# Kernel optimization log

Measured on AMD Instinct MI355X. Metric: run time of the kernel, lower is better.

## Reference

```python
import jax, jax.numpy as jnp
import numpy as np
from itertools import combinations

DIM = 3
METRIC = np.array([1.0, 1.0, 1.0], dtype=np.float32)
KERNEL_SIZE = 7
C_IN, C_OUT = 32, 32
HIDDEN = 64
NUM_LAYERS = 4
N_GRID = KERNEL_SIZE ** DIM


def _build_cayley(dim, metric):
    blades = [()] + [c for r in range(1, dim + 1) for c in combinations(range(dim), r)]
    idx = {b: i for i, b in enumerate(blades)}
    n = len(blades)
    C = np.zeros((n, n, n), dtype=np.float32)
    for i, a in enumerate(blades):
        for j, b in enumerate(blades):
            arr = list(a) + list(b)
            sign = 1.0
            changed = True
            while changed:
                changed = False
                t = 0
                while t < len(arr) - 1:
                    if arr[t] == arr[t + 1]:
                        sign *= metric[arr[t]]
                        del arr[t:t + 2]
                        changed = True
                        break
                    if arr[t] > arr[t + 1]:
                        arr[t], arr[t + 1] = arr[t + 1], arr[t]
                        sign = -sign
                        changed = True
                    t += 1
            C[i, j, idx[tuple(arr)]] = sign
    grades = np.array([len(b) for b in blades])
    return C, grades

_C_LRO, GRADES = _build_cayley(DIM, METRIC)
CAYLEY = np.transpose(_C_LRO, (0, 2, 1))  # [left, out, right] (CEGNN convention)
N_BLADES = CAYLEY.shape[0]
N_GRADES = DIM + 1

# nonzero grade-triple paths of the Cayley tensor and blade-level path-id lookup
_gp = np.zeros((N_GRADES,) * 3, dtype=bool)
for a in range(N_GRADES):
    for b in range(N_GRADES):
        for c in range(N_GRADES):
            _gp[a, b, c] = np.any(CAYLEY[np.ix_(GRADES == a, GRADES == b, GRADES == c)] != 0)
PATHS = np.argwhere(_gp)
P = len(PATHS)
assert P == 20  # product_paths_sum for Cl(3,0)
_pid = -np.ones((N_GRADES,) * 3, dtype=np.int64)
for p, (a, b, c) in enumerate(PATHS):
    _pid[a, b, c] = p
BLADE_PID = _pid[GRADES[:, None, None], GRADES[None, :, None], GRADES[None, None, :]]
BLADE_PID = np.where(BLADE_PID < 0, P, BLADE_PID)  # P -> zero slot

# centered relative-position grid, (N, 1, dim)
_ax = np.arange(KERNEL_SIZE, dtype=np.float32) - (KERNEL_SIZE - 1) / 2.0
_grid = np.stack(np.meshgrid(*([_ax] * DIM), indexing='ij'), axis=-1).reshape(-1, DIM)
REL_POS = jnp.asarray(_grid[:, None, :])
CAYLEY_J = jnp.asarray(CAYLEY)
GRADE_ONEHOT = jnp.asarray((GRADES[:, None] == np.arange(N_GRADES)[None, :]).astype(np.float32))
FACTOR = 1.0 / np.sqrt(float(KERNEL_SIZE ** DIM))
BLADES_OF = {g: np.where(GRADES == g)[0] for g in range(N_GRADES)}


def embed_grade(x, g):
    out = jnp.zeros(x.shape[:-1] + (N_BLADES,), x.dtype)
    return out.at[..., BLADES_OF[g]].set(x)


def expand_paths(w):
    # (..., P) grade-path weights -> (..., B, B, B) blade-level weights
    wz = jnp.concatenate([w, jnp.zeros(w.shape[:-1] + (1,), w.dtype)], axis=-1)
    return wz[..., BLADE_PID]


def mv_linear(x, W, b):
    # grade-wise equivariant channel mixing; x: (N,Ci,B), W: (G,Co,Ci), bias on scalar blade
    y = jnp.einsum('boi,nib->nob', W[GRADES], x)
    return y.at[:, :, 0].add(b)


def mv_silu(x, a, b):
    # gate each grade by sigmoid of its (learned-scaled) squared norm
    qg = jnp.einsum('ncb,bg->ncg', x * x, GRADE_ONEHOT)
    gate = jax.nn.sigmoid(a * qg + b)
    return x * gate[:, :, GRADES]


def gp_layer(x, w):
    # fully-connected steerable geometric product; x: (N,C,B), w: (Co,C,P)
    wc = expand_paths(w) * CAYLEY_J  # (Co, C, B, B, B)
    y = jnp.einsum('nik,oikjm,nim->noj', x, wc, x)
    return y / np.sqrt(float(x.shape[1]))


def setup_inputs() -> dict:
    key = jax.random.key(0)
    ks = jax.random.split(key, 8)
    G, B, H, Pn = N_GRADES, N_BLADES, HIDDEN, P
    rn = lambda k, s, sc: jax.random.normal(k, s, dtype=jnp.float32) * sc
    ci1 = C_IN + 1
    return {
        'condition': rn(ks[0], (C_IN, B), 1.0),
        'rel_pos_sigma': jnp.ones((1, 1, 1), jnp.float32),
        'cayley_w': rn(ks[1], (C_OUT, C_IN, Pn), 1.0 / np.sqrt(C_IN)),
        'lin0_W': rn(ks[2], (G, H, ci1), 1.0 / np.sqrt(ci1)),
        'lin0_b': jnp.zeros((H,), jnp.float32),
        'act0_a': rn(ks[3], (H, G), 0.2),
        'act0_b': jnp.zeros((H, G), jnp.float32),
        'gps_w': rn(ks[4], (NUM_LAYERS, H, H, Pn), 0.5 / np.sqrt(H)),
        'lins_W': rn(ks[5], (NUM_LAYERS - 1, G, H, H), 1.0 / np.sqrt(H)),
        'lins_b': jnp.zeros((NUM_LAYERS - 1, H), jnp.float32),
        'acts_a': rn(ks[6], (NUM_LAYERS - 1, H, G), 0.2),
        'acts_b': jnp.zeros((NUM_LAYERS - 1, H, G), jnp.float32),
        'out_W': rn(ks[7], (G, C_OUT * C_IN, H), 1.0 / np.sqrt(H)),
        'out_b': jnp.zeros((C_OUT * C_IN,), jnp.float32),
        'shell_sigma': jnp.ones((1, C_OUT, C_IN, B), jnp.float32),
    }


def reference(condition, rel_pos_sigma, cayley_w, lin0_W, lin0_b, act0_a, act0_b,
              gps_w, lins_W, lins_b, acts_a, acts_b, out_W, out_b, shell_sigma):
    metric = jnp.asarray(METRIC)
    q = jnp.sum(metric * REL_POS * REL_POS, axis=-1, keepdims=True)  # (N,1,1)
    scalar = jnp.exp(-q / (2.0 * rel_pos_sigma ** 2))
    x = embed_grade(scalar, 0) + embed_grade(REL_POS, 1)  # (N,1,B)
    cond = jnp.broadcast_to(condition[None], (N_GRID,) + condition.shape)
    x = jnp.concatenate([x, cond], axis=1)  # (N, c_in+1, B)
    # kernel network: CEGNN blocks [MVLinear -> MVSiLU -> steerable geometric product]
    h = gp_layer(mv_silu(mv_linear(x, lin0_W, lin0_b), act0_a, act0_b), gps_w[0])
    for l in range(NUM_LAYERS - 1):
        h = gp_layer(mv_silu(mv_linear(h, lins_W[l], lins_b[l]), acts_a[l], acts_b[l]), gps_w[l + 1])
    k = mv_linear(h, out_W, out_b).reshape(N_GRID, C_OUT, C_IN, N_BLADES)
    # per-(c_out,c_in,blade) scalar radial shell
    shell = jnp.exp(-q.reshape(N_GRID, 1, 1, 1) / (shell_sigma ** 2))
    k = k * shell * FACTOR
    # kernel head: sparse weighted-Cayley contraction
    wc = expand_paths(cayley_w) * CAYLEY_J  # (c_out, c_in, B, B, B)
    K = jnp.einsum('noik,oiklm->olimn', k, wc)
    return K.reshape(C_OUT * N_BLADES, C_IN * N_BLADES, KERNEL_SIZE, KERNEL_SIZE, KERNEL_SIZE)
```

## Files before the change

kernel.cpp:

```cpp
#include <hip/hip_runtime.h>
#include <math.h>

#define NB 8
#define NGRID 343
#define HID 64
#define NPATH 20

struct Tab {
  int prod_idx[8][8];
  int prod_sgn[8][8];
  int pid[4][4][4];
  int grade[8];
  int kk_idx[8][8];
  int kk_sgn[8][8];
};

constexpr Tab make_tab() {
  Tab t{};
  int mask[8]  = {0,1,2,4,3,5,6,7};
  int idxof[8] = {0,1,2,4,3,5,6,7};
  for (int k = 0; k < 8; ++k) {
    int g = 0;
    for (int b = 0; b < 3; ++b) g += (mask[k] >> b) & 1;
    t.grade[k] = g;
  }
  for (int k = 0; k < 8; ++k)
    for (int m = 0; m < 8; ++m) {
      int A = mask[k], B = mask[m];
      t.prod_idx[k][m] = idxof[A ^ B];
      int c = 0;
      for (int i = 0; i < 3; ++i)
        if ((B >> i) & 1)
          for (int j = i + 1; j < 3; ++j)
            if ((A >> j) & 1) c++;
      t.prod_sgn[k][m] = (c & 1) ? -1 : 1;
    }
  int pc = 0;
  for (int a = 0; a < 4; ++a)
    for (int b = 0; b < 4; ++b)
      for (int c = 0; c < 4; ++c) {
        bool ok = false;
        for (int k = 0; k < 8; ++k)
          for (int m = 0; m < 8; ++m)
            if (t.grade[k] == a && t.grade[m] == c &&
                t.grade[t.prod_idx[k][m]] == b)
              ok = true;
        t.pid[a][b][c] = ok ? pc++ : NPATH;
      }
  for (int l = 0; l < 8; ++l)
    for (int m = 0; m < 8; ++m)
      for (int k = 0; k < 8; ++k)
        if (t.prod_idx[k][m] == l) {
          t.kk_idx[l][m] = k;
          t.kk_sgn[l][m] = t.prod_sgn[k][m];
        }
  return t;
}
constexpr Tab TB = make_tab();

#define OFF_LIN0T 0
#define OFF_LINST 8448
#define OFF_GPST  57600
#define OFF_OUTWT 385280
#define OFF_KWS   647424

__global__ void ccs_prep_kernel(const float* __restrict__ lin0_W,
                                const float* __restrict__ lins_W,
                                const float* __restrict__ gps_w,
                                const float* __restrict__ out_W,
                                float* __restrict__ ws) {
  const int TOT = 8448 + 49152 + 327680 + 262144;
  for (int d = blockIdx.x * blockDim.x + threadIdx.x; d < TOT;
       d += gridDim.x * blockDim.x) {
    float v;
    if (d < 8448) {
      int idx = d;
      int hh = idx & 63, ch = (idx >> 6) % 33, g = (idx >> 6) / 33;
      v = lin0_W[(g * 64 + hh) * 33 + ch];
    } else if (d < 8448 + 49152) {
      int idx = d - OFF_LINST;
      int hh = idx & 63, i = (idx >> 6) & 63, g = (idx >> 12) & 3, l = idx >> 14;
      v = lins_W[((l * 4 + g) * 64 + hh) * 64 + i];
    } else if (d < 8448 + 49152 + 327680) {
      int idx = d - OFF_GPST;
      int o = idx & 63, p = (idx >> 6) % 20, i = ((idx >> 6) / 20) & 63,
          l = idx / 81920;
      v = gps_w[((l * 64 + o) * 64 + i) * 20 + p];
    } else {
      int idx = d - OFF_OUTWT;
      int oc = idx & 1023, i = (idx >> 10) & 63, g = idx >> 16;
      v = out_W[(g * 1024 + oc) * 64 + i];
    }
    ws[d] = v;
  }
}

__launch_bounds__(512)
__global__ void ccs_net_kernel(const float* __restrict__ condition,
                               const float* __restrict__ rel_pos_sigma,
                               const float* __restrict__ lin0_b,
                               const float* __restrict__ act0_a,
                               const float* __restrict__ act0_b,
                               const float* __restrict__ lins_b,
                               const float* __restrict__ acts_a,
                               const float* __restrict__ acts_b,
                               const float* __restrict__ out_b,
                               const float* __restrict__ shell_sigma,
                               const float* __restrict__ ws,
                               float* __restrict__ kws) {
  const float* lin0t = ws + OFF_LIN0T;
  const float* linst = ws + OFF_LINST;
  const float* gpst  = ws + OFF_GPST;
  const float* outwt = ws + OFF_OUTWT;

  __shared__ float xb[33 * 8];
  __shared__ float x0r[2][8];
  __shared__ __align__(16) float F0[2 * 512];
  __shared__ __align__(16) float F1[2 * 512];
  __shared__ float part[2 * 8 * 8 * 64];

  const int tid = threadIdx.x;
  const int n0 = blockIdx.x * 2;
  const int n1 = n0 + 1;

  const float sig = rel_pos_sigma[0];

  float qq[2];
  {
    int iz = n0 % 7, iy = (n0 / 7) % 7, ix = n0 / 49;
    float px = (float)ix - 3.f, py = (float)iy - 3.f, pz = (float)iz - 3.f;
    qq[0] = px * px + py * py + pz * pz;
  }
  {
    int nc = (n1 < NGRID) ? n1 : (NGRID - 1);
    int iz = nc % 7, iy = (nc / 7) % 7, ix = nc / 49;
    float px = (float)ix - 3.f, py = (float)iy - 3.f, pz = (float)iz - 3.f;
    qq[1] = px * px + py * py + pz * pz;
  }

  for (int t = tid; t < 264; t += 512) {
    int ch = t >> 3, b = t & 7;
    xb[t] = (ch == 0) ? 0.f : condition[(ch - 1) * 8 + b];
  }
  if (tid < 16) {
    int pt = tid >> 3, b = tid & 7;
    int nc = n0 + pt;
    if (nc >= NGRID) nc = NGRID - 1;
    int iz = nc % 7, iy = (nc / 7) % 7, ix = nc / 49;
    float px = (float)ix - 3.f, py = (float)iy - 3.f, pz = (float)iz - 3.f;
    float q = px * px + py * py + pz * pz;
    float scal = expf(-q / (2.f * sig * sig));
    x0r[pt][b] =
        (b == 0) ? scal : (b == 1) ? px : (b == 2) ? py : (b == 3) ? pz : 0.f;
  }
  __syncthreads();

  const int b8 = tid & 7;
  const int hh = (tid >> 3) & 63;
  const int gb = TB.grade[b8];

  {
    const float* wrow = lin0t + gb * 33 * 64 + hh;
    float w0 = wrow[0];
    float a0 = w0 * x0r[0][b8];
    float a1 = w0 * x0r[1][b8];
    if (b8 == 0) {
      float bb = lin0_b[hh];
      a0 += bb;
      a1 += bb;
    }
    #pragma unroll
    for (int ch = 1; ch < 33; ++ch) {
      float w = wrow[ch * 64];
      float xv = xb[ch * 8 + b8];
      a0 = fmaf(w, xv, a0);
      a1 = fmaf(w, xv, a1);
    }
    F0[hh * 8 + b8] = a0;
    F0[512 + hh * 8 + b8] = a1;
  }
  __syncthreads();

  auto silu = [&](const float* src, float* dst, const float* aa,
                  const float* bb) {
    int s0 = (gb == 0) ? 0 : (gb == 1) ? 1 : (gb == 2) ? 4 : 7;
    int cnt = (gb == 0 || gb == 3) ? 1 : 3;
    float A = aa[hh * 4 + gb], B = bb[hh * 4 + gb];
    #pragma unroll
    for (int pt = 0; pt < 2; ++pt) {
      float qg = 0.f;
      for (int u = 0; u < cnt; ++u) {
        float v = src[pt * 512 + hh * 8 + s0 + u];
        qg = fmaf(v, v, qg);
      }
      float z = fmaf(A, qg, B);
      float gate = 1.f / (1.f + expf(-z));
      dst[pt * 512 + hh * 8 + b8] = src[pt * 512 + hh * 8 + b8] * gate;
    }
  };

  auto lin = [&](const float* src, float* dst, const float* wt,
                 const float* bias) {
    const float* wrow = wt + gb * 64 * 64 + hh;
    float a0 = 0.f, a1 = 0.f;
    if (b8 == 0) {
      float bb = bias[hh];
      a0 = bb;
      a1 = bb;
    }
    #pragma unroll
    for (int i = 0; i < 64; ++i) {
      float w = wrow[i * 64];
      a0 = fmaf(w, src[i * 8 + b8], a0);
      a1 = fmaf(w, src[512 + i * 8 + b8], a1);
    }
    dst[hh * 8 + b8] = a0;
    dst[512 + hh * 8 + b8] = a1;
  };

  auto gp = [&](const float* src, float* dst, const float* wl) {
    const int o = tid & 63;
    const int isub = tid >> 6;
    float fa[8], fb[8];
    #pragma unroll
    for (int j = 0; j < 8; ++j) {
      fa[j] = 0.f;
      fb[j] = 0.f;
    }
    for (int it = 0; it < 8; ++it) {
      int i = isub * 8 + it;
      float4 va0 = *(const float4*)(src + i * 8);
      float4 va1 = *(const float4*)(src + i * 8 + 4);
      float4 vb0 = *(const float4*)(src + 512 + i * 8);
      float4 vb1 = *(const float4*)(src + 512 + i * 8 + 4);
      float xA[8] = {va0.x, va0.y, va0.z, va0.w, va1.x, va1.y, va1.z, va1.w};
      float xB[8] = {vb0.x, vb0.y, vb0.z, vb0.w, vb1.x, vb1.y, vb1.z, vb1.w};
      const float* wb = wl + i * 20 * 64 + o;
      float wp[20];
      #pragma unroll
      for (int p = 0; p < 20; ++p) wp[p] = wb[p * 64];
      #pragma unroll
      for (int k = 0; k < 8; ++k) {
        #pragma unroll
        for (int m = 0; m < 8; ++m) {
          const int j = TB.prod_idx[k][m];
          const int p = TB.pid[TB.grade[k]][TB.grade[j]][TB.grade[m]];
          if (TB.prod_sgn[k][m] > 0) {
            fa[j] = fmaf(xA[k] * xA[m], wp[p], fa[j]);
            fb[j] = fmaf(xB[k] * xB[m], wp[p], fb[j]);
          } else {
            fa[j] = fmaf(-xA[k] * xA[m], wp[p], fa[j]);
            fb[j] = fmaf(-xB[k] * xB[m], wp[p], fb[j]);
          }
        }
      }
    }
    #pragma unroll
    for (int j = 0; j < 8; ++j) {
      part[isub * 512 + j * 64 + o] = fa[j];
      part[4096 + isub * 512 + j * 64 + o] = fb[j];
    }
    __syncthreads();
    #pragma unroll
    for (int r = 0; r < 2; ++r) {
      int item = tid + r * 512;
      int oo = item & 63;
      int j = (item >> 6) & 7;
      int pt = item >> 9;
      const float* pp = part + pt * 4096 + j * 64 + oo;
      float s = pp[0] + pp[512] + pp[1024] + pp[1536] + pp[2048] + pp[2560] +
                pp[3072] + pp[3584];
      dst[pt * 512 + oo * 8 + j] = s * 0.125f;
    }
    __syncthreads();
  };

  silu(F0, F1, act0_a, act0_b);
  __syncthreads();
  gp(F1, F0, gpst + 0);

  float* f = F0;
  float* g_ = F1;
  for (int l = 0; l < 3; ++l) {
    lin(f, g_, linst + l * 16384, lins_b + l * 64);
    __syncthreads();
    silu(g_, f, acts_a + l * 256, acts_b + l * 256);
    __syncthreads();
    gp(f, g_, gpst + (l + 1) * 81920);
    float* t = f; f = g_; g_ = t;
  }

  const float FACTOR = 1.0f / sqrtf(343.0f);
  #pragma unroll
  for (int r = 0; r < 2; ++r) {
    int oc = tid + r * 512;
    float acc[2][8];
    #pragma unroll
    for (int pt = 0; pt < 2; ++pt)
      #pragma unroll
      for (int b = 0; b < 8; ++b) acc[pt][b] = 0.f;
    {
      float bb = out_b[oc];
      acc[0][0] = bb;
      acc[1][0] = bb;
    }
    #pragma unroll 4
    for (int i = 0; i < 64; ++i) {
      float w0 = outwt[(0 * 64 + i) * 1024 + oc];
      float w1 = outwt[(1 * 64 + i) * 1024 + oc];
      float w2 = outwt[(2 * 64 + i) * 1024 + oc];
      float w3 = outwt[(3 * 64 + i) * 1024 + oc];
      #pragma unroll
      for (int pt = 0; pt < 2; ++pt) {
        float4 h0 = *(const float4*)(f + pt * 512 + i * 8);
        float4 h1 = *(const float4*)(f + pt * 512 + i * 8 + 4);
        acc[pt][0] = fmaf(w0, h0.x, acc[pt][0]);
        acc[pt][1] = fmaf(w1, h0.y, acc[pt][1]);
        acc[pt][2] = fmaf(w1, h0.z, acc[pt][2]);
        acc[pt][3] = fmaf(w1, h0.w, acc[pt][3]);
        acc[pt][4] = fmaf(w2, h1.x, acc[pt][4]);
        acc[pt][5] = fmaf(w2, h1.y, acc[pt][5]);
        acc[pt][6] = fmaf(w2, h1.z, acc[pt][6]);
        acc[pt][7] = fmaf(w3, h1.w, acc[pt][7]);
      }
    }
    #pragma unroll
    for (int pt = 0; pt < 2; ++pt) {
      int n = n0 + pt;
      if (n < NGRID) {
        float q = qq[pt];
        float out8[8];
        #pragma unroll
        for (int b = 0; b < 8; ++b) {
          float ss = shell_sigma[oc * 8 + b];
          out8[b] = acc[pt][b] * expf(-q / (ss * ss)) * FACTOR;
        }
        float4* dstp = (float4*)(kws + ((size_t)oc * 343 + n) * 8);
        dstp[0] = make_float4(out8[0], out8[1], out8[2], out8[3]);
        dstp[1] = make_float4(out8[4], out8[5], out8[6], out8[7]);
      }
    }
  }
}

__launch_bounds__(64)
__global__ void ccs_expand_kernel(const float* __restrict__ cayley_w,
                                  const float* __restrict__ kws,
                                  float* __restrict__ out) {
  const int oi = blockIdx.x;
  const int o = oi >> 5, i = oi & 31;
  const int n = blockIdx.y * 64 + threadIdx.x;
  if (n >= NGRID) return;
  float cw[20];
  #pragma unroll
  for (int p = 0; p < 20; ++p) cw[p] = cayley_w[oi * 20 + p];
  const float* kp = kws + ((size_t)oi * 343 + n) * 8;
  float k8[8];
  #pragma unroll
  for (int b = 0; b < 8; ++b) k8[b] = kp[b];
  #pragma unroll
  for (int l = 0; l < 8; ++l) {
    #pragma unroll
    for (int m = 0; m < 8; ++m) {
      const int kk = TB.kk_idx[l][m];
      const int p = TB.pid[TB.grade[kk]][TB.grade[l]][TB.grade[m]];
      float v = k8[kk] * cw[p];
      if (TB.kk_sgn[l][m] < 0) v = -v;
      out[((size_t)((o * 8 + l) * 256 + i * 8 + m)) * 343 + n] = v;
    }
  }
}

extern "C" void kernel_launch(void* const* d_in, const int* in_sizes, int n_in,
                              void* d_out, int out_size, void* d_ws,
                              size_t ws_size, hipStream_t stream) {
  const float* condition     = (const float*)d_in[0];
  const float* rel_pos_sigma = (const float*)d_in[1];
  const float* cayley_w      = (const float*)d_in[2];
  const float* lin0_W        = (const float*)d_in[3];
  const float* lin0_b        = (const float*)d_in[4];
  const float* act0_a        = (const float*)d_in[5];
  const float* act0_b        = (const float*)d_in[6];
  const float* gps_w         = (const float*)d_in[7];
  const float* lins_W        = (const float*)d_in[8];
  const float* lins_b        = (const float*)d_in[9];
  const float* acts_a        = (const float*)d_in[10];
  const float* acts_b        = (const float*)d_in[11];
  const float* out_W         = (const float*)d_in[12];
  const float* out_b         = (const float*)d_in[13];
  const float* shell_sigma   = (const float*)d_in[14];

  float* ws = (float*)d_ws;
  float* kws = ws + OFF_KWS;
  float* out = (float*)d_out;

  ccs_prep_kernel<<<dim3(640), dim3(256), 0, stream>>>(lin0_W, lins_W, gps_w,
                                                       out_W, ws);
  ccs_net_kernel<<<dim3((NGRID + 1) / 2), dim3(512), 0, stream>>>(
      condition, rel_pos_sigma, lin0_b, act0_a, act0_b, lins_b, acts_a, acts_b,
      out_b, shell_sigma, ws, kws);
  ccs_expand_kernel<<<dim3(1024, 6), dim3(64), 0, stream>>>(cayley_w, kws, out);
}
```

Baseline: 229.8 us.

## Read weights in native layout with vectorized loads instead of transposing in prep

The prep kernel no longer transposes lins_W, gps_w and out_W into workspace; the net kernel reads them in their original row-major layout with float4 loads. This removes most of the prep kernel's traffic. A transposed copy of the activations (FT) is kept in shared memory so the linear layer can do float4 dot products per thread. The gp weights are double-buffered across iterations, and the output projection now handles two output channels per thread with vectorized weight loads. In exchange, lanes now read strided rows instead of coalesced columns, and there is extra shared-memory traffic and register pressure.

```diff
diff --git a/kernel.cpp b/kernel.cpp
--- a/kernel.cpp
+++ b/kernel.cpp
@@ -59,40 +59,14 @@
 constexpr Tab TB = make_tab();
 
 #define OFF_LIN0T 0
-#define OFF_LINST 8448
-#define OFF_GPST  57600
-#define OFF_OUTWT 385280
-#define OFF_KWS   647424
+#define OFF_KWS   9216
 
 __global__ void ccs_prep_kernel(const float* __restrict__ lin0_W,
-                                const float* __restrict__ lins_W,
-                                const float* __restrict__ gps_w,
-                                const float* __restrict__ out_W,
                                 float* __restrict__ ws) {
-  const int TOT = 8448 + 49152 + 327680 + 262144;
-  for (int d = blockIdx.x * blockDim.x + threadIdx.x; d < TOT;
-       d += gridDim.x * blockDim.x) {
-    float v;
-    if (d < 8448) {
-      int idx = d;
-      int hh = idx & 63, ch = (idx >> 6) % 33, g = (idx >> 6) / 33;
-      v = lin0_W[(g * 64 + hh) * 33 + ch];
-    } else if (d < 8448 + 49152) {
-      int idx = d - OFF_LINST;
-      int hh = idx & 63, i = (idx >> 6) & 63, g = (idx >> 12) & 3, l = idx >> 14;
-      v = lins_W[((l * 4 + g) * 64 + hh) * 64 + i];
-    } else if (d < 8448 + 49152 + 327680) {
-      int idx = d - OFF_GPST;
-      int o = idx & 63, p = (idx >> 6) % 20, i = ((idx >> 6) / 20) & 63,
-          l = idx / 81920;
-      v = gps_w[((l * 64 + o) * 64 + i) * 20 + p];
-    } else {
-      int idx = d - OFF_OUTWT;
-      int oc = idx & 1023, i = (idx >> 10) & 63, g = idx >> 16;
-      v = out_W[(g * 1024 + oc) * 64 + i];
-    }
-    ws[d] = v;
-  }
+  int d = blockIdx.x * blockDim.x + threadIdx.x;
+  if (d >= 9216) return;
+  int ch = d % 36, hh = (d / 36) & 63, g = d / 2304;
+  ws[d] = (ch < 33) ? lin0_W[(g * 64 + hh) * 33 + ch] : 0.f;
 }
 
 __launch_bounds__(512)
@@ -106,17 +80,18 @@
                                const float* __restrict__ acts_b,
                                const float* __restrict__ out_b,
                                const float* __restrict__ shell_sigma,
+                               const float* __restrict__ lins_W,
+                               const float* __restrict__ gps_w,
+                               const float* __restrict__ out_W,
                                const float* __restrict__ ws,
                                float* __restrict__ kws) {
   const float* lin0t = ws + OFF_LIN0T;
-  const float* linst = ws + OFF_LINST;
-  const float* gpst  = ws + OFF_GPST;
-  const float* outwt = ws + OFF_OUTWT;
 
   __shared__ float xb[33 * 8];
   __shared__ float x0r[2][8];
   __shared__ __align__(16) float F0[2 * 512];
   __shared__ __align__(16) float F1[2 * 512];
+  __shared__ __align__(16) float FT[2 * 512];
   __shared__ float part[2 * 8 * 8 * 64];
 
   const int tid = threadIdx.x;
@@ -160,10 +135,12 @@
   const int gb = TB.grade[b8];
 
   {
-    const float* wrow = lin0t + gb * 33 * 64 + hh;
-    float w0 = wrow[0];
-    float a0 = w0 * x0r[0][b8];
-    float a1 = w0 * x0r[1][b8];
+    const float4* w4 = (const float4*)(lin0t + (gb * 64 + hh) * 36);
+    float wv[36];
+    #pragma unroll
+    for (int t2 = 0; t2 < 9; ++t2) ((float4*)wv)[t2] = w4[t2];
+    float a0 = wv[0] * x0r[0][b8];
+    float a1 = wv[0] * x0r[1][b8];
     if (b8 == 0) {
       float bb = lin0_b[hh];
       a0 += bb;
@@ -171,10 +148,9 @@
     }
     #pragma unroll
     for (int ch = 1; ch < 33; ++ch) {
-      float w = wrow[ch * 64];
       float xv = xb[ch * 8 + b8];
-      a0 = fmaf(w, xv, a0);
-      a1 = fmaf(w, xv, a1);
+      a0 = fmaf(wv[ch], xv, a0);
+      a1 = fmaf(wv[ch], xv, a1);
     }
     F0[hh * 8 + b8] = a0;
     F0[512 + hh * 8 + b8] = a1;
@@ -199,9 +175,10 @@
     }
   };
 
-  auto lin = [&](const float* src, float* dst, const float* wt,
-                 const float* bias) {
-    const float* wrow = wt + gb * 64 * 64 + hh;
+  auto lin = [&](float* dst, const float* wt, const float* bias) {
+    const float4* w4 = (const float4*)(wt + gb * 4096 + hh * 64);
+    const float4* sA = (const float4*)(FT + b8 * 64);
+    const float4* sB = (const float4*)(FT + 512 + b8 * 64);
     float a0 = 0.f, a1 = 0.f;
     if (b8 == 0) {
       float bb = bias[hh];
@@ -209,10 +186,16 @@
       a1 = bb;
     }
     #pragma unroll
-    for (int i = 0; i < 64; ++i) {
-      float w = wrow[i * 64];
-      a0 = fmaf(w, src[i * 8 + b8], a0);
-      a1 = fmaf(w, src[512 + i * 8 + b8], a1);
+    for (int i4 = 0; i4 < 16; ++i4) {
+      float wv[4], xa[4], xbv[4];
+      *(float4*)wv = w4[i4];
+      *(float4*)xa = sA[i4];
+      *(float4*)xbv = sB[i4];
+      #pragma unroll
+      for (int u = 0; u < 4; ++u) {
+        a0 = fmaf(wv[u], xa[u], a0);
+        a1 = fmaf(wv[u], xbv[u], a1);
+      }
     }
     dst[hh * 8 + b8] = a0;
     dst[512 + hh * 8 + b8] = a1;
@@ -227,7 +210,19 @@
       fa[j] = 0.f;
       fb[j] = 0.f;
     }
+    const float4* wb4 =
+        (const float4*)(wl + (size_t)o * 1280 + (size_t)isub * 160);
+    float4 wq[5];
+    #pragma unroll
+    for (int t2 = 0; t2 < 5; ++t2) wq[t2] = wb4[t2];
+    #pragma unroll
     for (int it = 0; it < 8; ++it) {
+      float4 wn[5];
+      if (it < 7) {
+        const float4* nb = wb4 + (it + 1) * 5;
+        #pragma unroll
+        for (int t2 = 0; t2 < 5; ++t2) wn[t2] = nb[t2];
+      }
       int i = isub * 8 + it;
       float4 va0 = *(const float4*)(src + i * 8);
       float4 va1 = *(const float4*)(src + i * 8 + 4);
@@ -235,10 +230,9 @@
       float4 vb1 = *(const float4*)(src + 512 + i * 8 + 4);
       float xA[8] = {va0.x, va0.y, va0.z, va0.w, va1.x, va1.y, va1.z, va1.w};
       float xB[8] = {vb0.x, vb0.y, vb0.z, vb0.w, vb1.x, vb1.y, vb1.z, vb1.w};
-      const float* wb = wl + i * 20 * 64 + o;
       float wp[20];
       #pragma unroll
-      for (int p = 0; p < 20; ++p) wp[p] = wb[p * 64];
+      for (int t2 = 0; t2 < 5; ++t2) ((float4*)wp)[t2] = wq[t2];
       #pragma unroll
       for (int k = 0; k < 8; ++k) {
         #pragma unroll
@@ -254,6 +248,10 @@
           }
         }
       }
+      if (it < 7) {
+        #pragma unroll
+        for (int t2 = 0; t2 < 5; ++t2) wq[t2] = wn[t2];
+      }
     }
     #pragma unroll
     for (int j = 0; j < 8; ++j) {
@@ -270,74 +268,94 @@
       const float* pp = part + pt * 4096 + j * 64 + oo;
       float s = pp[0] + pp[512] + pp[1024] + pp[1536] + pp[2048] + pp[2560] +
                 pp[3072] + pp[3584];
-      dst[pt * 512 + oo * 8 + j] = s * 0.125f;
+      s *= 0.125f;
+      dst[pt * 512 + oo * 8 + j] = s;
+      FT[pt * 512 + j * 64 + oo] = s;
     }
     __syncthreads();
   };
 
   silu(F0, F1, act0_a, act0_b);
   __syncthreads();
-  gp(F1, F0, gpst + 0);
+  gp(F1, F0, gps_w + 0);
 
   float* f = F0;
   float* g_ = F1;
   for (int l = 0; l < 3; ++l) {
-    lin(f, g_, linst + l * 16384, lins_b + l * 64);
+    lin(g_, lins_W + l * 16384, lins_b + l * 64);
     __syncthreads();
     silu(g_, f, acts_a + l * 256, acts_b + l * 256);
     __syncthreads();
-    gp(f, g_, gpst + (l + 1) * 81920);
+    gp(f, g_, gps_w + (size_t)(l + 1) * 81920);
     float* t = f; f = g_; g_ = t;
   }
 
   const float FACTOR = 1.0f / sqrtf(343.0f);
-  #pragma unroll
-  for (int r = 0; r < 2; ++r) {
-    int oc = tid + r * 512;
-    float acc[2][8];
-    #pragma unroll
-    for (int pt = 0; pt < 2; ++pt)
-      #pragma unroll
-      for (int b = 0; b < 8; ++b) acc[pt][b] = 0.f;
+  {
+    const int oc0 = tid;
+    const int oc1 = tid + 512;
+    float acc[2][2][8];
+    #pragma unroll
+    for (int r2 = 0; r2 < 2; ++r2)
+      #pragma unroll
+      for (int pt = 0; pt < 2; ++pt)
+        #pragma unroll
+        for (int b = 0; b < 8; ++b) acc[r2][pt][b] = 0.f;
     {
-      float bb = out_b[oc];
-      acc[0][0] = bb;
-      acc[1][0] = bb;
-    }
+      float b0 = out_b[oc0], b1 = out_b[oc1];
+      acc[0][0][0] = b0; acc[0][1][0] = b0;
+      acc[1][0][0] = b1; acc[1][1][0] = b1;
+    }
+    const float4* ow4 = (const float4*)out_W;
     #pragma unroll 4
-    for (int i = 0; i < 64; ++i) {
-      float w0 = outwt[(0 * 64 + i) * 1024 + oc];
-      float w1 = outwt[(1 * 64 + i) * 1024 + oc];
-      float w2 = outwt[(2 * 64 + i) * 1024 + oc];
-      float w3 = outwt[(3 * 64 + i) * 1024 + oc];
+    for (int i4 = 0; i4 < 16; ++i4) {
+      float w[2][4][4];
+      #pragma unroll
+      for (int g = 0; g < 4; ++g) {
+        *(float4*)w[0][g] = ow4[((size_t)g * 1024 + oc0) * 16 + i4];
+        *(float4*)w[1][g] = ow4[((size_t)g * 1024 + oc1) * 16 + i4];
+      }
+      #pragma unroll
+      for (int u = 0; u < 4; ++u) {
+        int i = i4 * 4 + u;
+        #pragma unroll
+        for (int pt = 0; pt < 2; ++pt) {
+          float h[8];
+          *(float4*)h = *(const float4*)(f + pt * 512 + i * 8);
+          *(float4*)(h + 4) = *(const float4*)(f + pt * 512 + i * 8 + 4);
+          #pragma unroll
+          for (int r2 = 0; r2 < 2; ++r2) {
+            acc[r2][pt][0] = fmaf(w[r2][0][u], h[0], acc[r2][pt][0]);
+            acc[r2][pt][1] = fmaf(w[r2][1][u], h[1], acc[r2][pt][1]);
+            acc[r2][pt][2] = fmaf(w[r2][1][u], h[2], acc[r2][pt][2]);
+            acc[r2][pt][3] = fmaf(w[r2][1][u], h[3], acc[r2][pt][3]);
+            acc[r2][pt][4] = fmaf(w[r2][2][u], h[4], acc[r2][pt][4]);
+            acc[r2][pt][5] = fmaf(w[r2][2][u], h[5], acc[r2][pt][5]);
+            acc[r2][pt][6] = fmaf(w[r2][2][u], h[6], acc[r2][pt][6]);
+            acc[r2][pt][7] = fmaf(w[r2][3][u], h[7], acc[r2][pt][7]);
+          }
+        }
+      }
+    }
+    #pragma unroll
+    for (int r2 = 0; r2 < 2; ++r2) {
+      int oc = tid + r2 * 512;
+      float sh[8];
+      *(float4*)sh = *(const float4*)(shell_sigma + oc * 8);
+      *(float4*)(sh + 4) = *(const float4*)(shell_sigma + oc * 8 + 4);
       #pragma unroll
       for (int pt = 0; pt < 2; ++pt) {
-        float4 h0 = *(const float4*)(f + pt * 512 + i * 8);
-        float4 h1 = *(const float4*)(f + pt * 512 + i * 8 + 4);
-        acc[pt][0] = fmaf(w0, h0.x, acc[pt][0]);
-        acc[pt][1] = fmaf(w1, h0.y, acc[pt][1]);
-        acc[pt][2] = fmaf(w1, h0.z, acc[pt][2]);
-        acc[pt][3] = fmaf(w1, h0.w, acc[pt][3]);
-        acc[pt][4] = fmaf(w2, h1.x, acc[pt][4]);
-        acc[pt][5] = fmaf(w2, h1.y, acc[pt][5]);
-        acc[pt][6] = fmaf(w2, h1.z, acc[pt][6]);
-        acc[pt][7] = fmaf(w3, h1.w, acc[pt][7]);
-      }
-    }
-    #pragma unroll
-    for (int pt = 0; pt < 2; ++pt) {
-      int n = n0 + pt;
-      if (n < NGRID) {
-        float q = qq[pt];
-        float out8[8];
-        #pragma unroll
-        for (int b = 0; b < 8; ++b) {
-          float ss = shell_sigma[oc * 8 + b];
-          out8[b] = acc[pt][b] * expf(-q / (ss * ss)) * FACTOR;
+        int n = n0 + pt;
+        if (n < NGRID) {
+          float q = qq[pt];
+          float out8[8];
+          #pragma unroll
+          for (int b = 0; b < 8; ++b)
+            out8[b] = acc[r2][pt][b] * expf(-q / (sh[b] * sh[b])) * FACTOR;
+          float4* dstp = (float4*)(kws + ((size_t)oc * 343 + n) * 8);
+          dstp[0] = make_float4(out8[0], out8[1], out8[2], out8[3]);
+          dstp[1] = make_float4(out8[4], out8[5], out8[6], out8[7]);
         }
-        float4* dstp = (float4*)(kws + ((size_t)oc * 343 + n) * 8);
-        dstp[0] = make_float4(out8[0], out8[1], out8[2], out8[3]);
-        dstp[1] = make_float4(out8[4], out8[5], out8[6], out8[7]);
       }
     }
   }
@@ -352,12 +370,17 @@
   const int n = blockIdx.y * 64 + threadIdx.x;
   if (n >= NGRID) return;
   float cw[20];
-  #pragma unroll
-  for (int p = 0; p < 20; ++p) cw[p] = cayley_w[oi * 20 + p];
-  const float* kp = kws + ((size_t)oi * 343 + n) * 8;
+  {
+    const float4* c4 = (const float4*)(cayley_w + oi * 20);
+    #pragma unroll
+    for (int t2 = 0; t2 < 5; ++t2) ((float4*)cw)[t2] = c4[t2];
+  }
   float k8[8];
-  #pragma unroll
-  for (int b = 0; b < 8; ++b) k8[b] = kp[b];
+  {
+    const float4* kp4 = (const float4*)(kws + ((size_t)oi * 343 + n) * 8);
+    *(float4*)k8 = kp4[0];
+    *(float4*)(k8 + 4) = kp4[1];
+  }
   #pragma unroll
   for (int l = 0; l < 8; ++l) {
     #pragma unroll
@@ -394,10 +417,9 @@
   float* kws = ws + OFF_KWS;
   float* out = (float*)d_out;
 
-  ccs_prep_kernel<<<dim3(640), dim3(256), 0, stream>>>(lin0_W, lins_W, gps_w,
-                                                       out_W, ws);
+  ccs_prep_kernel<<<dim3(36), dim3(256), 0, stream>>>(lin0_W, ws);
   ccs_net_kernel<<<dim3((NGRID + 1) / 2), dim3(512), 0, stream>>>(
       condition, rel_pos_sigma, lin0_b, act0_a, act0_b, lins_b, acts_a, acts_b,
-      out_b, shell_sigma, ws, kws);
+      out_b, shell_sigma, lins_W, gps_w, out_W, ws, kws);
   ccs_expand_kernel<<<dim3(1024, 6), dim3(64), 0, stream>>>(cayley_w, kws, out);
 }
```

New measurement: 256.7 us. +11.7%, slower.

## Double net kernel block size to 1024 threads, split points and input-channel slices

Applied to the files above, without the earlier changes.

The network kernel now runs 1024 threads per block. Each thread handles one grid point in the linear and SiLU stages instead of two, the geometric-product stage splits input channels into 16 slices of 4 instead of 8 slices of 8, and the output projection gives each thread one output channel. The geometric-product weights for the next input channel are prefetched into registers, and a few scalar loads become float4 loads. This raises per-block parallelism and latency hiding on the serial per-point chain. In exchange the partial-sum buffer in shared memory doubles and the reduction grows to 16 terms, and the larger block with its launch-bound hint may increase register pressure or spilling.

```diff
diff --git a/kernel.cpp b/kernel.cpp
--- a/kernel.cpp
+++ b/kernel.cpp
@@ -95,7 +95,7 @@
   }
 }
 
-__launch_bounds__(512)
+__launch_bounds__(1024, 4)
 __global__ void ccs_net_kernel(const float* __restrict__ condition,
                                const float* __restrict__ rel_pos_sigma,
                                const float* __restrict__ lin0_b,
@@ -117,7 +117,7 @@
   __shared__ float x0r[2][8];
   __shared__ __align__(16) float F0[2 * 512];
   __shared__ __align__(16) float F1[2 * 512];
-  __shared__ float part[2 * 8 * 8 * 64];
+  __shared__ float part[2 * 16 * 8 * 64];
 
   const int tid = threadIdx.x;
   const int n0 = blockIdx.x * 2;
@@ -138,7 +138,7 @@
     qq[1] = px * px + py * py + pz * pz;
   }
 
-  for (int t = tid; t < 264; t += 512) {
+  for (int t = tid; t < 264; t += 1024) {
     int ch = t >> 3, b = t & 7;
     xb[t] = (ch == 0) ? 0.f : condition[(ch - 1) * 8 + b];
   }
@@ -155,29 +155,20 @@
   }
   __syncthreads();
 
-  const int b8 = tid & 7;
-  const int hh = (tid >> 3) & 63;
+  const int pt = tid >> 9;
+  const int idx = tid & 511;
+  const int b8 = idx & 7;
+  const int hh = idx >> 3;
   const int gb = TB.grade[b8];
 
   {
     const float* wrow = lin0t + gb * 33 * 64 + hh;
-    float w0 = wrow[0];
-    float a0 = w0 * x0r[0][b8];
-    float a1 = w0 * x0r[1][b8];
-    if (b8 == 0) {
-      float bb = lin0_b[hh];
-      a0 += bb;
-      a1 += bb;
-    }
-    #pragma unroll
-    for (int ch = 1; ch < 33; ++ch) {
-      float w = wrow[ch * 64];
-      float xv = xb[ch * 8 + b8];
-      a0 = fmaf(w, xv, a0);
-      a1 = fmaf(w, xv, a1);
-    }
-    F0[hh * 8 + b8] = a0;
-    F0[512 + hh * 8 + b8] = a1;
+    float a = wrow[0] * x0r[pt][b8];
+    if (b8 == 0) a += lin0_b[hh];
+    #pragma unroll
+    for (int ch = 1; ch < 33; ++ch)
+      a = fmaf(wrow[ch * 64], xb[ch * 8 + b8], a);
+    F0[pt * 512 + hh * 8 + b8] = a;
   }
   __syncthreads();
 
@@ -186,36 +177,24 @@
     int s0 = (gb == 0) ? 0 : (gb == 1) ? 1 : (gb == 2) ? 4 : 7;
     int cnt = (gb == 0 || gb == 3) ? 1 : 3;
     float A = aa[hh * 4 + gb], B = bb[hh * 4 + gb];
-    #pragma unroll
-    for (int pt = 0; pt < 2; ++pt) {
-      float qg = 0.f;
-      for (int u = 0; u < cnt; ++u) {
-        float v = src[pt * 512 + hh * 8 + s0 + u];
-        qg = fmaf(v, v, qg);
-      }
-      float z = fmaf(A, qg, B);
-      float gate = 1.f / (1.f + expf(-z));
-      dst[pt * 512 + hh * 8 + b8] = src[pt * 512 + hh * 8 + b8] * gate;
-    }
+    float qg = 0.f;
+    for (int u = 0; u < cnt; ++u) {
+      float v = src[pt * 512 + hh * 8 + s0 + u];
+      qg = fmaf(v, v, qg);
+    }
+    float z = fmaf(A, qg, B);
+    float gate = 1.f / (1.f + expf(-z));
+    dst[pt * 512 + hh * 8 + b8] = src[pt * 512 + hh * 8 + b8] * gate;
   };
 
   auto lin = [&](const float* src, float* dst, const float* wt,
                  const float* bias) {
     const float* wrow = wt + gb * 64 * 64 + hh;
-    float a0 = 0.f, a1 = 0.f;
-    if (b8 == 0) {
-      float bb = bias[hh];
-      a0 = bb;
-      a1 = bb;
-    }
-    #pragma unroll
-    for (int i = 0; i < 64; ++i) {
-      float w = wrow[i * 64];
-      a0 = fmaf(w, src[i * 8 + b8], a0);
-      a1 = fmaf(w, src[512 + i * 8 + b8], a1);
-    }
-    dst[hh * 8 + b8] = a0;
-    dst[512 + hh * 8 + b8] = a1;
+    float a = (b8 == 0) ? bias[hh] : 0.f;
+    #pragma unroll
+    for (int i = 0; i < 64; ++i)
+      a = fmaf(wrow[i * 64], src[pt * 512 + i * 8 + b8], a);
+    dst[pt * 512 + hh * 8 + b8] = a;
   };
 
   auto gp = [&](const float* src, float* dst, const float* wl) {
@@ -227,18 +206,23 @@
       fa[j] = 0.f;
       fb[j] = 0.f;
     }
-    for (int it = 0; it < 8; ++it) {
-      int i = isub * 8 + it;
+    const float* wb = wl + (size_t)(isub * 4) * 1280 + o;
+    float wp[20], wn[20];
+    #pragma unroll
+    for (int p = 0; p < 20; ++p) wp[p] = wb[p * 64];
+    for (int it = 0; it < 4; ++it) {
+      if (it < 3) {
+        const float* nb = wb + (it + 1) * 1280;
+        #pragma unroll
+        for (int p = 0; p < 20; ++p) wn[p] = nb[p * 64];
+      }
+      int i = isub * 4 + it;
       float4 va0 = *(const float4*)(src + i * 8);
       float4 va1 = *(const float4*)(src + i * 8 + 4);
       float4 vb0 = *(const float4*)(src + 512 + i * 8);
       float4 vb1 = *(const float4*)(src + 512 + i * 8 + 4);
       float xA[8] = {va0.x, va0.y, va0.z, va0.w, va1.x, va1.y, va1.z, va1.w};
       float xB[8] = {vb0.x, vb0.y, vb0.z, vb0.w, vb1.x, vb1.y, vb1.z, vb1.w};
-      const float* wb = wl + i * 20 * 64 + o;
-      float wp[20];
-      #pragma unroll
-      for (int p = 0; p < 20; ++p) wp[p] = wb[p * 64];
       #pragma unroll
       for (int k = 0; k < 8; ++k) {
         #pragma unroll
@@ -254,23 +238,26 @@
           }
         }
       }
+      if (it < 3) {
+        #pragma unroll
+        for (int p = 0; p < 20; ++p) wp[p] = wn[p];
+      }
     }
     #pragma unroll
     for (int j = 0; j < 8; ++j) {
       part[isub * 512 + j * 64 + o] = fa[j];
-      part[4096 + isub * 512 + j * 64 + o] = fb[j];
+      part[8192 + isub * 512 + j * 64 + o] = fb[j];
     }
     __syncthreads();
-    #pragma unroll
-    for (int r = 0; r < 2; ++r) {
-      int item = tid + r * 512;
-      int oo = item & 63;
-      int j = (item >> 6) & 7;
-      int pt = item >> 9;
-      const float* pp = part + pt * 4096 + j * 64 + oo;
-      float s = pp[0] + pp[512] + pp[1024] + pp[1536] + pp[2048] + pp[2560] +
-                pp[3072] + pp[3584];
-      dst[pt * 512 + oo * 8 + j] = s * 0.125f;
+    {
+      int oo = tid & 63;
+      int j = (tid >> 6) & 7;
+      int pp_ = tid >> 9;
+      const float* pp = part + pp_ * 8192 + j * 64 + oo;
+      float s = 0.f;
+      #pragma unroll
+      for (int is = 0; is < 16; ++is) s += pp[is * 512];
+      dst[pp_ * 512 + oo * 8 + j] = s * 0.125f;
     }
     __syncthreads();
   };
@@ -286,55 +273,56 @@
     __syncthreads();
     silu(g_, f, acts_a + l * 256, acts_b + l * 256);
     __syncthreads();
-    gp(f, g_, gpst + (l + 1) * 81920);
+    gp(f, g_, gpst + (size_t)(l + 1) * 81920);
     float* t = f; f = g_; g_ = t;
   }
 
   const float FACTOR = 1.0f / sqrtf(343.0f);
-  #pragma unroll
-  for (int r = 0; r < 2; ++r) {
-    int oc = tid + r * 512;
+  {
+    const int oc = tid;
     float acc[2][8];
     #pragma unroll
-    for (int pt = 0; pt < 2; ++pt)
+    for (int p2 = 0; p2 < 2; ++p2)
       #pragma unroll
-      for (int b = 0; b < 8; ++b) acc[pt][b] = 0.f;
+      for (int b = 0; b < 8; ++b) acc[p2][b] = 0.f;
     {
       float bb = out_b[oc];
       acc[0][0] = bb;
       acc[1][0] = bb;
     }
-    #pragma unroll 4
+    #pragma unroll 8
     for (int i = 0; i < 64; ++i) {
       float w0 = outwt[(0 * 64 + i) * 1024 + oc];
       float w1 = outwt[(1 * 64 + i) * 1024 + oc];
       float w2 = outwt[(2 * 64 + i) * 1024 + oc];
       float w3 = outwt[(3 * 64 + i) * 1024 + oc];
       #pragma unroll
-      for (int pt = 0; pt < 2; ++pt) {
-        float4 h0 = *(const float4*)(f + pt * 512 + i * 8);
-        float4 h1 = *(const float4*)(f + pt * 512 + i * 8 + 4);
-        acc[pt][0] = fmaf(w0, h0.x, acc[pt][0]);
-        acc[pt][1] = fmaf(w1, h0.y, acc[pt][1]);
-        acc[pt][2] = fmaf(w1, h0.z, acc[pt][2]);
-        acc[pt][3] = fmaf(w1, h0.w, acc[pt][3]);
-        acc[pt][4] = fmaf(w2, h1.x, acc[pt][4]);
-        acc[pt][5] = fmaf(w2, h1.y, acc[pt][5]);
-        acc[pt][6] = fmaf(w2, h1.z, acc[pt][6]);
-        acc[pt][7] = fmaf(w3, h1.w, acc[pt][7]);
-      }
-    }
-    #pragma unroll
-    for (int pt = 0; pt < 2; ++pt) {
-      int n = n0 + pt;
+      for (int p2 = 0; p2 < 2; ++p2) {
+        float h[8];
+        *(float4*)h = *(const float4*)(f + p2 * 512 + i * 8);
+        *(float4*)(h + 4) = *(const float4*)(f + p2 * 512 + i * 8 + 4);
+        acc[p2][0] = fmaf(w0, h[0], acc[p2][0]);
+        acc[p2][1] = fmaf(w1, h[1], acc[p2][1]);
+        acc[p2][2] = fmaf(w1, h[2], acc[p2][2]);
+        acc[p2][3] = fmaf(w1, h[3], acc[p2][3]);
+        acc[p2][4] = fmaf(w2, h[4], acc[p2][4]);
+        acc[p2][5] = fmaf(w2, h[5], acc[p2][5]);
+        acc[p2][6] = fmaf(w2, h[6], acc[p2][6]);
+        acc[p2][7] = fmaf(w3, h[7], acc[p2][7]);
+      }
+    }
+    float sh[8];
+    *(float4*)sh = *(const float4*)(shell_sigma + oc * 8);
+    *(float4*)(sh + 4) = *(const float4*)(shell_sigma + oc * 8 + 4);
+    #pragma unroll
+    for (int p2 = 0; p2 < 2; ++p2) {
+      int n = n0 + p2;
       if (n < NGRID) {
-        float q = qq[pt];
+        float q = qq[p2];
         float out8[8];
         #pragma unroll
-        for (int b = 0; b < 8; ++b) {
-          float ss = shell_sigma[oc * 8 + b];
-          out8[b] = acc[pt][b] * expf(-q / (ss * ss)) * FACTOR;
-        }
+        for (int b = 0; b < 8; ++b)
+          out8[b] = acc[p2][b] * expf(-q / (sh[b] * sh[b])) * FACTOR;
         float4* dstp = (float4*)(kws + ((size_t)oc * 343 + n) * 8);
         dstp[0] = make_float4(out8[0], out8[1], out8[2], out8[3]);
         dstp[1] = make_float4(out8[4], out8[5], out8[6], out8[7]);
@@ -354,10 +342,12 @@
   float cw[20];
   #pragma unroll
   for (int p = 0; p < 20; ++p) cw[p] = cayley_w[oi * 20 + p];
-  const float* kp = kws + ((size_t)oi * 343 + n) * 8;
   float k8[8];
-  #pragma unroll
-  for (int b = 0; b < 8; ++b) k8[b] = kp[b];
+  {
+    const float4* kp4 = (const float4*)(kws + ((size_t)oi * 343 + n) * 8);
+    *(float4*)k8 = kp4[0];
+    *(float4*)(k8 + 4) = kp4[1];
+  }
   #pragma unroll
   for (int l = 0; l < 8; ++l) {
     #pragma unroll
@@ -396,7 +386,7 @@
 
   ccs_prep_kernel<<<dim3(640), dim3(256), 0, stream>>>(lin0_W, lins_W, gps_w,
                                                        out_W, ws);
-  ccs_net_kernel<<<dim3((NGRID + 1) / 2), dim3(512), 0, stream>>>(
+  ccs_net_kernel<<<dim3((NGRID + 1) / 2), dim3(1024), 0, stream>>>(
       condition, rel_pos_sigma, lin0_b, act0_a, act0_b, lins_b, acts_a, acts_b,
       out_b, shell_sigma, ws, kws);
   ccs_expand_kernel<<<dim3(1024, 6), dim3(64), 0, stream>>>(cayley_w, kws, out);
```

Measured after the change: 258.5 us. +12.5%, slower.

## Stage geometric-product weights through double-buffered LDS with register prefetch

Applied to the files above, without the earlier changes.

The geometric-product layer now streams each layer's weights in eight chunks. Each chunk goes from global memory into registers and then into a double-buffered shared-memory buffer, so the next chunk's global load overlaps the current chunk's compute. This replaces the per-thread strided global weight reads and changes which input rows each wave handles. Smaller changes add a min-blocks hint to launch bounds, raise the unroll on the output projection, and vectorise the shell_sigma and kws loads. The extra 80KB of LDS plus two syncs per chunk may limit occupancy, which conflicts with the 2-blocks hint.

```diff
diff --git a/kernel.cpp b/kernel.cpp
--- a/kernel.cpp
+++ b/kernel.cpp
@@ -95,7 +95,7 @@
   }
 }
 
-__launch_bounds__(512)
+__launch_bounds__(512, 2)
 __global__ void ccs_net_kernel(const float* __restrict__ condition,
                                const float* __restrict__ rel_pos_sigma,
                                const float* __restrict__ lin0_b,
@@ -118,6 +118,7 @@
   __shared__ __align__(16) float F0[2 * 512];
   __shared__ __align__(16) float F1[2 * 512];
   __shared__ float part[2 * 8 * 8 * 64];
+  __shared__ __align__(16) float wbuf[2 * 10240];
 
   const int tid = threadIdx.x;
   const int n0 = blockIdx.x * 2;
@@ -220,25 +221,50 @@
 
   auto gp = [&](const float* src, float* dst, const float* wl) {
     const int o = tid & 63;
-    const int isub = tid >> 6;
+    const int w = tid >> 6;
     float fa[8], fb[8];
     #pragma unroll
     for (int j = 0; j < 8; ++j) {
       fa[j] = 0.f;
       fb[j] = 0.f;
     }
-    for (int it = 0; it < 8; ++it) {
-      int i = isub * 8 + it;
+    const float4* gsrc = (const float4*)wl;
+    float4 rg0, rg1, rg2, rg3, rg4;
+    rg0 = gsrc[tid];
+    rg1 = gsrc[tid + 512];
+    rg2 = gsrc[tid + 1024];
+    rg3 = gsrc[tid + 1536];
+    rg4 = gsrc[tid + 2048];
+    for (int c = 0; c < 8; ++c) {
+      __syncthreads();
+      {
+        float4* wb4 = (float4*)(wbuf + (c & 1) * 10240);
+        wb4[tid] = rg0;
+        wb4[tid + 512] = rg1;
+        wb4[tid + 1024] = rg2;
+        wb4[tid + 1536] = rg3;
+        wb4[tid + 2048] = rg4;
+      }
+      if (c < 7) {
+        const float4* gn = gsrc + (c + 1) * 2560;
+        rg0 = gn[tid];
+        rg1 = gn[tid + 512];
+        rg2 = gn[tid + 1024];
+        rg3 = gn[tid + 1536];
+        rg4 = gn[tid + 2048];
+      }
+      __syncthreads();
+      const int i = c * 8 + w;
+      const float* wp_l = wbuf + (c & 1) * 10240 + w * 1280 + o;
+      float wp[20];
+      #pragma unroll
+      for (int p = 0; p < 20; ++p) wp[p] = wp_l[p * 64];
       float4 va0 = *(const float4*)(src + i * 8);
       float4 va1 = *(const float4*)(src + i * 8 + 4);
       float4 vb0 = *(const float4*)(src + 512 + i * 8);
       float4 vb1 = *(const float4*)(src + 512 + i * 8 + 4);
       float xA[8] = {va0.x, va0.y, va0.z, va0.w, va1.x, va1.y, va1.z, va1.w};
       float xB[8] = {vb0.x, vb0.y, vb0.z, vb0.w, vb1.x, vb1.y, vb1.z, vb1.w};
-      const float* wb = wl + i * 20 * 64 + o;
-      float wp[20];
-      #pragma unroll
-      for (int p = 0; p < 20; ++p) wp[p] = wb[p * 64];
       #pragma unroll
       for (int k = 0; k < 8; ++k) {
         #pragma unroll
@@ -257,8 +283,8 @@
     }
     #pragma unroll
     for (int j = 0; j < 8; ++j) {
-      part[isub * 512 + j * 64 + o] = fa[j];
-      part[4096 + isub * 512 + j * 64 + o] = fb[j];
+      part[w * 512 + j * 64 + o] = fa[j];
+      part[4096 + w * 512 + j * 64 + o] = fb[j];
     }
     __syncthreads();
     #pragma unroll
@@ -286,7 +312,7 @@
     __syncthreads();
     silu(g_, f, acts_a + l * 256, acts_b + l * 256);
     __syncthreads();
-    gp(f, g_, gpst + (l + 1) * 81920);
+    gp(f, g_, gpst + (size_t)(l + 1) * 81920);
     float* t = f; f = g_; g_ = t;
   }
 
@@ -304,7 +330,7 @@
       acc[0][0] = bb;
       acc[1][0] = bb;
     }
-    #pragma unroll 4
+    #pragma unroll 8
     for (int i = 0; i < 64; ++i) {
       float w0 = outwt[(0 * 64 + i) * 1024 + oc];
       float w1 = outwt[(1 * 64 + i) * 1024 + oc];
@@ -312,18 +338,22 @@
       float w3 = outwt[(3 * 64 + i) * 1024 + oc];
       #pragma unroll
       for (int pt = 0; pt < 2; ++pt) {
-        float4 h0 = *(const float4*)(f + pt * 512 + i * 8);
-        float4 h1 = *(const float4*)(f + pt * 512 + i * 8 + 4);
-        acc[pt][0] = fmaf(w0, h0.x, acc[pt][0]);
-        acc[pt][1] = fmaf(w1, h0.y, acc[pt][1]);
-        acc[pt][2] = fmaf(w1, h0.z, acc[pt][2]);
-        acc[pt][3] = fmaf(w1, h0.w, acc[pt][3]);
-        acc[pt][4] = fmaf(w2, h1.x, acc[pt][4]);
-        acc[pt][5] = fmaf(w2, h1.y, acc[pt][5]);
-        acc[pt][6] = fmaf(w2, h1.z, acc[pt][6]);
-        acc[pt][7] = fmaf(w3, h1.w, acc[pt][7]);
-      }
-    }
+        float h[8];
+        *(float4*)h = *(const float4*)(f + pt * 512 + i * 8);
+        *(float4*)(h + 4) = *(const float4*)(f + pt * 512 + i * 8 + 4);
+        acc[pt][0] = fmaf(w0, h[0], acc[pt][0]);
+        acc[pt][1] = fmaf(w1, h[1], acc[pt][1]);
+        acc[pt][2] = fmaf(w1, h[2], acc[pt][2]);
+        acc[pt][3] = fmaf(w1, h[3], acc[pt][3]);
+        acc[pt][4] = fmaf(w2, h[4], acc[pt][4]);
+        acc[pt][5] = fmaf(w2, h[5], acc[pt][5]);
+        acc[pt][6] = fmaf(w2, h[6], acc[pt][6]);
+        acc[pt][7] = fmaf(w3, h[7], acc[pt][7]);
+      }
+    }
+    float sh[8];
+    *(float4*)sh = *(const float4*)(shell_sigma + oc * 8);
+    *(float4*)(sh + 4) = *(const float4*)(shell_sigma + oc * 8 + 4);
     #pragma unroll
     for (int pt = 0; pt < 2; ++pt) {
       int n = n0 + pt;
@@ -331,10 +361,8 @@
         float q = qq[pt];
         float out8[8];
         #pragma unroll
-        for (int b = 0; b < 8; ++b) {
-          float ss = shell_sigma[oc * 8 + b];
-          out8[b] = acc[pt][b] * expf(-q / (ss * ss)) * FACTOR;
-        }
+        for (int b = 0; b < 8; ++b)
+          out8[b] = acc[pt][b] * expf(-q / (sh[b] * sh[b])) * FACTOR;
         float4* dstp = (float4*)(kws + ((size_t)oc * 343 + n) * 8);
         dstp[0] = make_float4(out8[0], out8[1], out8[2], out8[3]);
         dstp[1] = make_float4(out8[4], out8[5], out8[6], out8[7]);
@@ -354,10 +382,12 @@
   float cw[20];
   #pragma unroll
   for (int p = 0; p < 20; ++p) cw[p] = cayley_w[oi * 20 + p];
-  const float* kp = kws + ((size_t)oi * 343 + n) * 8;
   float k8[8];
-  #pragma unroll
-  for (int b = 0; b < 8; ++b) k8[b] = kp[b];
+  {
+    const float4* kp4 = (const float4*)(kws + ((size_t)oi * 343 + n) * 8);
+    *(float4*)k8 = kp4[0];
+    *(float4*)(k8 + 4) = kp4[1];
+  }
   #pragma unroll
   for (int l = 0; l < 8; ++l) {
     #pragma unroll
```

Result: slower. 236.5 us (+2.9%).
